# Kernel optimization log

Measured on AMD Instinct MI355X. Metric: run time of the kernel, lower is better.

Reference implementation:

```python
import jax, jax.numpy as jnp
import numpy as np

N = 100000  # nodes

def gcn_layer(x, W, b, src, dst, norm):
    # x: [N, Fin] -> [N, Fout]; symmetric-normalized aggregation (PyG GCNConv)
    h = x @ W                                   # linear first (no bias yet)
    msg = h[src] * norm[:, None]                # gather + edge-wise scale
    out = jax.ops.segment_sum(msg, dst, num_segments=N)  # scatter-add to targets
    return out + b

def _prep_edges(edge_index):
    # add self loops
    loops = jnp.arange(N, dtype=edge_index.dtype)
    src = jnp.concatenate([edge_index[0], loops])
    dst = jnp.concatenate([edge_index[1], loops])
    # deg computed on target nodes with unit edge weights
    deg = jax.ops.segment_sum(jnp.ones_like(dst, dtype=jnp.float32), dst, num_segments=N)
    dinv = jnp.where(deg > 0, jax.lax.rsqrt(deg), 0.0)
    norm = dinv[src] * dinv[dst]
    return src, dst, norm

def setup_inputs() -> dict:
    key = jax.random.key(0)
    ks = jax.random.split(key, 8)
    F_in, H1, H2, C = 512, 256, 64, 10
    E = 3200000
    x = jax.random.normal(ks[0], (N, F_in), dtype=jnp.float32)
    edge_index = jax.random.randint(ks[1], (2, E), 0, N, dtype=jnp.int64)
    def glorot(k, fan_in, fan_out):
        s = jnp.sqrt(6.0 / (fan_in + fan_out))
        return jax.random.uniform(k, (fan_in, fan_out), jnp.float32, -s, s)
    return {
        "x": x,
        "edge_index": edge_index,
        "W1": glorot(ks[2], F_in, H1), "b1": jnp.zeros((H1,), jnp.float32),
        "W2": glorot(ks[3], H1, H2),   "b2": jnp.zeros((H2,), jnp.float32),
        "W3": glorot(ks[4], H2, C),    "b3": jnp.zeros((C,), jnp.float32),
    }

def reference(x, edge_index, W1, b1, W2, b2, W3, b3):
    src, dst, norm = _prep_edges(edge_index)
    h = jax.nn.relu(gcn_layer(x, W1, b1, src, dst, norm))
    h = jax.nn.relu(gcn_layer(h, W2, b2, src, dst, norm))
    h = gcn_layer(h, W3, b3, src, dst, norm)
    return jax.nn.log_softmax(h, axis=1)
```

## Files before the change

### kernel.cpp

```cpp
#include <hip/hip_runtime.h>
#include <math.h>

#define NNODES 100000
#define NEDGES 3200000
#define NB 391
#define PB 512
#define CHUNK 6250

typedef __attribute__((ext_vector_type(4))) float f32x4;
typedef __attribute__((ext_vector_type(2))) float f32x2;
typedef __attribute__((ext_vector_type(8))) short bf16x8;

__device__ __forceinline__ float bf2f(ushort u) {
    union { unsigned u; float f; } v; v.u = ((unsigned)u) << 16; return v.f;
}
__device__ __forceinline__ ushort f2bf(float f) {
    union { float f; unsigned u; } v; v.f = f;
    unsigned r = v.u + 0x7FFFu + ((v.u >> 16) & 1u);
    return (ushort)(r >> 16);
}

__device__ __forceinline__ unsigned pack_bf2(float f0, float f1) {
    union { float f; unsigned u; } a, b; a.f = f0; b.f = f1;
#if __has_builtin(__builtin_amdgcn_perm)
    return __builtin_amdgcn_perm(b.u, a.u, 0x07060302u);
#else
    return (b.u & 0xFFFF0000u) | (a.u >> 16);
#endif
}

#if __has_builtin(__builtin_amdgcn_cvt_pk_fp8_f32) && __has_builtin(__builtin_amdgcn_cvt_pk_f32_fp8)
#define FP8_HW 1
#else
#define FP8_HW 0
#endif

__device__ __forceinline__ unsigned fp8enc_sw(float f) {
    union { float f; unsigned u; } v; v.f = f;
    unsigned sign = v.u >> 31;
    float a = fabsf(f);
    if (a >= 448.0f) return (sign << 7) | 0x7E;
    if (a < 0.0009765625f) return sign << 7;
    unsigned u = v.u & 0x7FFFFFFFu;
    u += 0x7FFFFu + ((u >> 20) & 1u);
    int e2 = (int)(u >> 23) - 127;
    if (e2 < -6) {
        int m = (int)(a * 512.0f + 0.5f); if (m > 7) m = 7;
        return (sign << 7) | (unsigned)m;
    }
    if (e2 > 8) return (sign << 7) | 0x7E;
    unsigned mant = (u >> 20) & 7u;
    return (sign << 7) | ((unsigned)(e2 + 7) << 3) | mant;
}
__device__ __forceinline__ float fp8dec_sw(unsigned b) {
    unsigned s = b >> 7, e = (b >> 3) & 0xF, m = b & 7;
    float v;
    if (e == 0) v = (float)m * 0.001953125f;
    else { union { unsigned u; float f; } x; x.u = ((e + 120u) << 23) | (m << 20); v = x.f; }
    return s ? -v : v;
}

__device__ __forceinline__ unsigned char f2fp8(float f) {
#if FP8_HW
    return (unsigned char)(__builtin_amdgcn_cvt_pk_fp8_f32(f, 0.f, 0, false) & 0xFF);
#else
    return (unsigned char)fp8enc_sw(f);
#endif
}
__device__ __forceinline__ void fp8x4_acc2(unsigned w, f32x2& a01, f32x2& a23) {
#if FP8_HW
    a01 += __builtin_amdgcn_cvt_pk_f32_fp8((int)w, false);
    a23 += __builtin_amdgcn_cvt_pk_f32_fp8((int)w, true);
#else
    a01[0] += fp8dec_sw(w & 0xFF); a01[1] += fp8dec_sw((w >> 8) & 0xFF);
    a23[0] += fp8dec_sw((w >> 16) & 0xFF); a23[1] += fp8dec_sw(w >> 24);
#endif
}

__global__ void bucket_hist(const int* __restrict__ dst, int e, int* __restrict__ hist) {
    __shared__ int h[NB];
    const int b = blockIdx.x, t = threadIdx.x;
    for (int j = t; j < NB; j += 256) h[j] = 0;
    __syncthreads();
    const int lo = b * CHUNK;
    int hi = lo + CHUNK; if (hi > e) hi = e;
    for (int i = lo + t; i < hi; i += 256)
        atomicAdd(&h[dst[i] >> 8], 1);
    __syncthreads();
    for (int j = t; j < NB; j += 256) hist[b * NB + j] = h[j];
}

__global__ void scan_buckets(int* __restrict__ hist, int* __restrict__ btotal) {
    __shared__ int s[256];
    const int j = blockIdx.x, t = threadIdx.x;
    int v0 = hist[(2 * t) * NB + j];
    int v1 = hist[(2 * t + 1) * NB + j];
    int p = v0 + v1;
    s[t] = p;
    __syncthreads();
    for (int off = 1; off < 256; off <<= 1) {
        int u = (t >= off) ? s[t - off] : 0;
        __syncthreads();
        s[t] += u;
        __syncthreads();
    }
    int excl = s[t] - p;
    hist[(2 * t) * NB + j] = excl;
    hist[(2 * t + 1) * NB + j] = excl + v0;
    if (t == 255) btotal[j] = s[255];
}

__global__ void scan_btotal(const int* __restrict__ btotal, int* __restrict__ bstart, int e) {
    __shared__ int s[512];
    const int t = threadIdx.x;
    int v = (t < NB) ? btotal[t] : 0;
    s[t] = v;
    __syncthreads();
    for (int off = 1; off < 512; off <<= 1) {
        int u = (t >= off) ? s[t - off] : 0;
        __syncthreads();
        s[t] += u;
        __syncthreads();
    }
    if (t < NB) bstart[t] = s[t] - v;
    if (t == 0) bstart[NB] = e;
}

__global__ void bucket_scatter(const int* __restrict__ src, const int* __restrict__ dst, int e,
                               const int* __restrict__ hist, const int* __restrict__ bstart,
                               unsigned* __restrict__ bucketed) {
    __shared__ int off[NB];
    const int b = blockIdx.x, t = threadIdx.x;
    for (int j = t; j < NB; j += 256) off[j] = bstart[j] + hist[b * NB + j];
    __syncthreads();
    const int lo = b * CHUNK;
    int hi = lo + CHUNK; if (hi > e) hi = e;
    for (int i = lo + t; i < hi; i += 256) {
        int d = dst[i];
        int j = d >> 8;
        int p = atomicAdd(&off[j], 1);
        bucketed[p] = (unsigned)src[i] | ((unsigned)(d & 255) << 24);
    }
}

__global__ void bucket_finalize(const unsigned* __restrict__ bucketed, const int* __restrict__ bstart,
                                float* __restrict__ dinv, int* __restrict__ rowptr,
                                int* __restrict__ esrc, int n, int e) {
    __shared__ int h[256];
    __shared__ int s[256];
    __shared__ int rp[256];
    const int j = blockIdx.x, t = threadIdx.x;
    h[t] = 0;
    __syncthreads();
    const int lo = bstart[j], hi = bstart[j + 1];
    for (int i = lo + t; i < hi; i += 256)
        atomicAdd(&h[bucketed[i] >> 24], 1);
    __syncthreads();
    const int c = h[t] + 1;
    s[t] = c;
    __syncthreads();
    for (int off = 1; off < 256; off <<= 1) {
        int u = (t >= off) ? s[t - off] : 0;
        __syncthreads();
        s[t] += u;
        __syncthreads();
    }
    const int excl = s[t] - c;
    const int base = j << 8;
    const int node = base + t;
    const int myrp = bstart[j] + base + excl;
    rp[t] = myrp;
    if (node < n) {
        dinv[node] = rsqrtf((float)c);
        rowptr[node] = myrp;
        esrc[myrp] = node;
    }
    if (j == 0 && t == 0) rowptr[n] = e + n;
    h[t] = 0;
    __syncthreads();
    for (int i = lo + t; i < hi; i += 256) {
        unsigned ed = bucketed[i];
        int l = ed >> 24;
        int off = atomicAdd(&h[l], 1);
        esrc[rp[l] + 1 + off] = (int)(ed & 0xFFFFFFu);
    }
}

__global__ void conv_wt(const float* __restrict__ W, ushort* __restrict__ Wt,
                        int K, int N, int Npad) {
    int idx = blockIdx.x * blockDim.x + threadIdx.x;
    if (idx >= Npad * K) return;
    int n = idx / K, k = idx % K;
    Wt[idx] = (n < N) ? f2bf(W[(size_t)k * N + n]) : (ushort)0;
}

__global__ void conv_wt8(const float* __restrict__ W, unsigned char* __restrict__ Wt,
                         int K, int N, int Npad) {
    int idx = blockIdx.x * blockDim.x + threadIdx.x;
    if (idx >= Npad * K) return;
    int n = idx / K, k = idx % K;
    Wt[idx] = (n < N) ? f2fp8(W[(size_t)k * N + n]) : (unsigned char)0;
}

template <int BM, int BN, int BK, int WM, int WN>
__launch_bounds__(WM* WN * 64)
__global__ void gemm_f32a(const float* __restrict__ A, const ushort* __restrict__ Bt,
                          const float* __restrict__ dinv, unsigned char* __restrict__ Cout,
                          int M, int N, int K) {
    constexpr int NT = WM * WN * 64;
    __shared__ __align__(16) float Asf[BM][BK];
    __shared__ __align__(16) ushort Bs[BN][BK];
    const int tid = threadIdx.x;
    const int wid = tid >> 6, lane = tid & 63;
    const int wr = wid / WN, wc = wid % WN;
    constexpr int TM = BM / WM, TN = BN / WN;
    constexpr int FM = TM / 16, FN = TN / 16;
    const int m0 = blockIdx.y * BM, n0 = blockIdx.x * BN;
    const int ln = lane & 15, ks4 = (lane >> 4) * 2;

    f32x4 acc[FM][FN] = {};

    constexpr int CPRA = BK / 4;
    constexpr int ACH = BM * CPRA;
    constexpr int CPRB = BK / 8;
    constexpr int BCH = BN * CPRB;

    for (int k0 = 0; k0 < K; k0 += BK) {
        #pragma unroll
        for (int it = 0; it < ACH / NT; ++it) {
            int c = it * NT + tid;
            int row = c >> 3, chs = c & 7;
            int gch = chs ^ (row & 7);
            int gm = m0 + row; if (gm >= M) gm = M - 1;
            const float* gp = &A[(size_t)gm * K + k0 + gch * 4];
            __builtin_amdgcn_global_load_lds(
                (const __attribute__((address_space(1))) void*)gp,
                (__attribute__((address_space(3))) void*)((char*)&Asf[0][0] + c * 16),
                16, 0, 0);
        }
        #pragma unroll
        for (int it = 0; it < BCH / NT; ++it) {
            int c = it * NT + tid;
            int row = c / CPRB, ch = c % CPRB;
            const ushort* gp = &Bt[(size_t)(n0 + row) * K + k0 + ch * 8];
            __builtin_amdgcn_global_load_lds(
                (const __attribute__((address_space(1))) void*)gp,
                (__attribute__((address_space(3))) void*)((char*)&Bs[0][0] + c * 16),
                16, 0, 0);
        }
        __syncthreads();

        bf16x8 af[FM], bfr[FN];
        #pragma unroll
        for (int mi = 0; mi < FM; ++mi) {
            int r = wr * TM + mi * 16 + ln;
            const char* rowp = (const char*)&Asf[0][0] + r * (BK * 4);
            float4 a0 = *(const float4*)(rowp + ((ks4 ^ (r & 7)) * 16));
            float4 a1 = *(const float4*)(rowp + (((ks4 + 1) ^ (r & 7)) * 16));
            union { unsigned w[4]; bf16x8 v; } u;
            u.w[0] = pack_bf2(a0.x, a0.y);
            u.w[1] = pack_bf2(a0.z, a0.w);
            u.w[2] = pack_bf2(a1.x, a1.y);
            u.w[3] = pack_bf2(a1.z, a1.w);
            af[mi] = u.v;
        }
        const int ks = (lane >> 4) * 8;
        #pragma unroll
        for (int nj = 0; nj < FN; ++nj)
            bfr[nj] = *(const bf16x8*)&Bs[wc * TN + nj * 16 + ln][ks];
        #pragma unroll
        for (int mi = 0; mi < FM; ++mi)
            #pragma unroll
            for (int nj = 0; nj < FN; ++nj)
                acc[mi][nj] = __builtin_amdgcn_mfma_f32_16x16x32_bf16(af[mi], bfr[nj], acc[mi][nj], 0, 0, 0);
        __syncthreads();
    }

    const int rbase = (lane >> 4) * 4;
    #pragma unroll
    for (int mi = 0; mi < FM; ++mi) {
        #pragma unroll
        for (int r = 0; r < 4; ++r) {
            int gm = m0 + wr * TM + mi * 16 + rbase + r;
            if (gm >= M) continue;
            float d = dinv[gm];
            #pragma unroll
            for (int nj = 0; nj < FN; ++nj) {
                int gn = n0 + wc * TN + nj * 16 + ln;
                Cout[(size_t)gm * N + gn] = f2fp8(acc[mi][nj][r] * d);
            }
        }
    }
}

template <int BM, int BN, int BK, int WM, int WN, int OUTK>
__launch_bounds__(WM* WN * 64)
__global__ void gemm_fp8(const unsigned char* __restrict__ A, const unsigned char* __restrict__ Bt,
                         const float* __restrict__ dinv, void* __restrict__ Cout,
                         int M, int N, int K) {
    constexpr int NT = WM * WN * 64;
    __shared__ __align__(16) unsigned char As[BM][BK];
    __shared__ __align__(16) unsigned char Bs[BN][BK];
    const int tid = threadIdx.x;
    const int wid = tid >> 6, lane = tid & 63;
    const int wr = wid / WN, wc = wid % WN;
    constexpr int TM = BM / WM, TN = BN / WN;
    constexpr int FM = TM / 16, FN = TN / 16;
    const int m0 = blockIdx.y * BM, n0 = blockIdx.x * BN;
    const int ln = lane & 15;

    f32x4 acc[FM][FN] = {};

    constexpr int CPR = BK / 16;
    constexpr int ACH = BM * CPR;
    constexpr int BCH = BN * CPR;

    for (int k0 = 0; k0 < K; k0 += BK) {
        #pragma unroll
        for (int it = 0; it < (ACH + NT - 1) / NT; ++it) {
            int c = it * NT + tid;
            if ((ACH % NT == 0) || (c < ACH)) {
                int row = c / CPR, ch = c % CPR;
                int gm = m0 + row; if (gm >= M) gm = M - 1;
                const unsigned char* gp = &A[(size_t)gm * K + k0 + ch * 16];
                __builtin_amdgcn_global_load_lds(
                    (const __attribute__((address_space(1))) void*)gp,
                    (__attribute__((address_space(3))) void*)((char*)&As[0][0] + c * 16),
                    16, 0, 0);
            }
        }
        #pragma unroll
        for (int it = 0; it < (BCH + NT - 1) / NT; ++it) {
            int c = it * NT + tid;
            if ((BCH % NT == 0) || (c < BCH)) {
                int row = c / CPR, ch = c % CPR;
                const unsigned char* gp = &Bt[(size_t)(n0 + row) * K + k0 + ch * 16];
                __builtin_amdgcn_global_load_lds(
                    (const __attribute__((address_space(1))) void*)gp,
                    (__attribute__((address_space(3))) void*)((char*)&Bs[0][0] + c * 16),
                    16, 0, 0);
            }
        }
        __syncthreads();

        long af[FM], bfr[FN];
        #pragma unroll
        for (int mi = 0; mi < FM; ++mi)
            af[mi] = ((const long*)&As[0][0])[(wr * TM + mi * 16 + ln) * (BK / 8) + (lane >> 4)];
        #pragma unroll
        for (int nj = 0; nj < FN; ++nj)
            bfr[nj] = ((const long*)&Bs[0][0])[(wc * TN + nj * 16 + ln) * (BK / 8) + (lane >> 4)];
        #pragma unroll
        for (int mi = 0; mi < FM; ++mi)
            #pragma unroll
            for (int nj = 0; nj < FN; ++nj)
                acc[mi][nj] = __builtin_amdgcn_mfma_f32_16x16x32_fp8_fp8(af[mi], bfr[nj], acc[mi][nj], 0, 0, 0);
        __syncthreads();
    }

    const int rbase = (lane >> 4) * 4;
    #pragma unroll
    for (int mi = 0; mi < FM; ++mi) {
        #pragma unroll
        for (int r = 0; r < 4; ++r) {
            int gm = m0 + wr * TM + mi * 16 + rbase + r;
            if (gm >= M) continue;
            float d = dinv[gm];
            #pragma unroll
            for (int nj = 0; nj < FN; ++nj) {
                int gn = n0 + wc * TN + nj * 16 + ln;
                float v = acc[mi][nj][r] * d;
                if (OUTK == 0) ((ushort*)Cout)[(size_t)gm * N + gn] = f2bf(v);
                else           ((unsigned char*)Cout)[(size_t)gm * N + gn] = f2fp8(v);
            }
        }
    }
}

__global__ void agg1_fp8(const unsigned* __restrict__ h, const int* __restrict__ rowptr,
                         const int* __restrict__ esrc, const float* __restrict__ dinv,
                         const float* __restrict__ bias, unsigned char* __restrict__ out, int n) {
    const int wid = threadIdx.x >> 6, lane = threadIdx.x & 63;
    const int i = blockIdx.x * 4 + wid;
    if (i >= n) return;
    const int lo = rowptr[i], hi = rowptr[i + 1];
    f32x2 a01 = {0.f, 0.f}, a23 = {0.f, 0.f};
    int e = lo;
    for (; e + 7 < hi; e += 8) {
        int s[8];
        unsigned w[8];
        #pragma unroll
        for (int q = 0; q < 8; ++q) s[q] = esrc[e + q];
        #pragma unroll
        for (int q = 0; q < 8; ++q) w[q] = h[(size_t)s[q] * 64 + lane];
        #pragma unroll
        for (int q = 0; q < 8; ++q) fp8x4_acc2(w[q], a01, a23);
    }
    for (; e < hi; ++e)
        fp8x4_acc2(h[(size_t)esrc[e] * 64 + lane], a01, a23);

    float d = dinv[i];
    const int f0 = lane * 4;
    float4 b = *(const float4*)&bias[f0];
    uchar4 o;
    o.x = f2fp8(fmaxf(a01[0] * d + b.x, 0.f));
    o.y = f2fp8(fmaxf(a01[1] * d + b.y, 0.f));
    o.z = f2fp8(fmaxf(a23[0] * d + b.z, 0.f));
    o.w = f2fp8(fmaxf(a23[1] * d + b.w, 0.f));
    *(uchar4*)&out[(size_t)i * 256 + f0] = o;
}

__global__ void agg2_fp8(const unsigned* __restrict__ h, const int* __restrict__ rowptr,
                         const int* __restrict__ esrc, const float* __restrict__ dinv,
                         const float* __restrict__ bias, unsigned char* __restrict__ out, int n) {
    const int g = threadIdx.x >> 4, j = threadIdx.x & 15;
    const int i = blockIdx.x * 16 + g;
    if (i >= n) return;
    const int lo = rowptr[i], hi = rowptr[i + 1];
    f32x2 a01 = {0.f, 0.f}, a23 = {0.f, 0.f};
    int e = lo;
    for (; e + 3 < hi; e += 4) {
        int s0 = esrc[e], s1 = esrc[e + 1], s2 = esrc[e + 2], s3 = esrc[e + 3];
        unsigned w0 = h[(size_t)s0 * 16 + j];
        unsigned w1 = h[(size_t)s1 * 16 + j];
        unsigned w2 = h[(size_t)s2 * 16 + j];
        unsigned w3 = h[(size_t)s3 * 16 + j];
        fp8x4_acc2(w0, a01, a23);
        fp8x4_acc2(w1, a01, a23);
        fp8x4_acc2(w2, a01, a23);
        fp8x4_acc2(w3, a01, a23);
    }
    for (; e < hi; ++e)
        fp8x4_acc2(h[(size_t)esrc[e] * 16 + j], a01, a23);

    float d = dinv[i];
    const int f0 = j * 4;
    float4 b = *(const float4*)&bias[f0];
    uchar4 o;
    o.x = f2fp8(fmaxf(a01[0] * d + b.x, 0.f));
    o.y = f2fp8(fmaxf(a01[1] * d + b.y, 0.f));
    o.z = f2fp8(fmaxf(a23[0] * d + b.z, 0.f));
    o.w = f2fp8(fmaxf(a23[1] * d + b.w, 0.f));
    *(uchar4*)&out[(size_t)i * 64 + f0] = o;
}

__global__ void agg3_logsoftmax(const ushort* __restrict__ h3, const int* __restrict__ rowptr,
                                const int* __restrict__ esrc, const float* __restrict__ dinv,
                                const float* __restrict__ bias, float* __restrict__ out, int n) {
    const int g = threadIdx.x >> 3, j = threadIdx.x & 7;
    const int i = blockIdx.x * 32 + g;
    if (i >= n) return;
    const int lo = rowptr[i], hi = rowptr[i + 1];
    float a0 = 0.f, a1 = 0.f;
    int e = lo;
    for (; e + 3 < hi; e += 4) {
        int s0 = esrc[e], s1 = esrc[e + 1], s2 = esrc[e + 2], s3 = esrc[e + 3];
        unsigned w0 = *(const unsigned*)&h3[(size_t)s0 * 16 + 2 * j];
        unsigned w1 = *(const unsigned*)&h3[(size_t)s1 * 16 + 2 * j];
        unsigned w2 = *(const unsigned*)&h3[(size_t)s2 * 16 + 2 * j];
        unsigned w3 = *(const unsigned*)&h3[(size_t)s3 * 16 + 2 * j];
        a0 += bf2f((ushort)(w0 & 0xFFFF)) + bf2f((ushort)(w1 & 0xFFFF))
            + bf2f((ushort)(w2 & 0xFFFF)) + bf2f((ushort)(w3 & 0xFFFF));
        a1 += bf2f((ushort)(w0 >> 16)) + bf2f((ushort)(w1 >> 16))
            + bf2f((ushort)(w2 >> 16)) + bf2f((ushort)(w3 >> 16));
    }
    for (; e < hi; ++e) {
        unsigned w = *(const unsigned*)&h3[(size_t)esrc[e] * 16 + 2 * j];
        a0 += bf2f((ushort)(w & 0xFFFF));
        a1 += bf2f((ushort)(w >> 16));
    }
    const int f0 = 2 * j;
    float d = dinv[i];
    float v0 = (f0 < 10) ? (a0 * d + bias[f0]) : -INFINITY;
    float v1 = (f0 + 1 < 10) ? (a1 * d + bias[f0 + 1]) : -INFINITY;
    float m = fmaxf(v0, v1);
    #pragma unroll
    for (int off = 1; off < 8; off <<= 1) m = fmaxf(m, __shfl_xor(m, off, 8));
    float ex = ((f0 < 10) ? expf(v0 - m) : 0.f) + ((f0 + 1 < 10) ? expf(v1 - m) : 0.f);
    #pragma unroll
    for (int off = 1; off < 8; off <<= 1) ex += __shfl_xor(ex, off, 8);
    float ls = logf(ex);
    if (f0 < 10)     out[(size_t)i * 10 + f0] = v0 - m - ls;
    if (f0 + 1 < 10) out[(size_t)i * 10 + f0 + 1] = v1 - m - ls;
}

extern "C" void kernel_launch(void* const* d_in, const int* in_sizes, int n_in,
                              void* d_out, int out_size, void* d_ws, size_t ws_size,
                              hipStream_t stream) {
    const int N = NNODES, E = NEDGES;
    const float* x  = (const float*)d_in[0];
    const int*   ei = (const int*)d_in[1];
    const float* W1 = (const float*)d_in[2];
    const float* b1 = (const float*)d_in[3];
    const float* W2 = (const float*)d_in[4];
    const float* b2 = (const float*)d_in[5];
    const float* W3 = (const float*)d_in[6];
    const float* b3 = (const float*)d_in[7];
    float* out = (float*)d_out;
    const int* src = ei;
    const int* dst = ei + E;

    char* ws = (char*)d_ws;
    size_t off = 0;
    auto alloc = [&](size_t bytes) -> void* {
        void* p = ws + off;
        off = (off + bytes + 255) & ~(size_t)255;
        return p;
    };
    float* dinv   = (float*)alloc((size_t)N * 4);
    int*   rowptr = (int*)alloc((size_t)(N + 1) * 4);
    int*   btotal = (int*)alloc((size_t)NB * 4);
    int*   bstart = (int*)alloc((size_t)(NB + 1) * 4);
    int*   esrc   = (int*)alloc((size_t)(E + N) * 4);
    ushort* W1t   = (ushort*)alloc((size_t)256 * 512 * 2);
    unsigned char* W2t8 = (unsigned char*)alloc((size_t)64 * 256);
    unsigned char* W3t8 = (unsigned char*)alloc((size_t)16 * 64);
    ushort* h3b   = (ushort*)alloc((size_t)N * 16 * 2);
    ushort* buf1  = (ushort*)alloc((size_t)N * 256 * 2);
    ushort* buf2  = (ushort*)alloc((size_t)N * 256 * 2);
    int*   hist   = (int*)buf1;
    unsigned* bucketed = (unsigned*)buf2;
    unsigned char* h1fp8 = (unsigned char*)buf1;
    unsigned char* a1fp8 = (unsigned char*)buf2;
    unsigned char* h2fp8 = (unsigned char*)buf1;
    unsigned char* a2fp8 = (unsigned char*)buf2;

    const int T = 256;
    bucket_hist<<<PB, T, 0, stream>>>(dst, E, hist);
    scan_buckets<<<NB, T, 0, stream>>>(hist, btotal);
    scan_btotal<<<1, 512, 0, stream>>>(btotal, bstart, E);
    bucket_scatter<<<PB, T, 0, stream>>>(src, dst, E, hist, bstart, bucketed);
    bucket_finalize<<<NB, T, 0, stream>>>(bucketed, bstart, dinv, rowptr, esrc, N, E);

    conv_wt<<<(256 * 512 + T - 1) / T, T, 0, stream>>>(W1, W1t, 512, 256, 256);
    conv_wt8<<<(64 * 256 + T - 1) / T, T, 0, stream>>>(W2, W2t8, 256, 64, 64);
    conv_wt8<<<(16 * 64 + T - 1) / T, T, 0, stream>>>(W3, W3t8, 64, 10, 16);

    const int MB = (N + 127) / 128;

    gemm_f32a<128, 256, 32, 2, 4><<<dim3(1, MB), 512, 0, stream>>>(x, W1t, dinv, h1fp8, N, 256, 512);
    agg1_fp8<<<(N + 3) / 4, 256, 0, stream>>>((const unsigned*)h1fp8, rowptr, esrc, dinv, b1, a1fp8, N);

    gemm_fp8<128, 64, 32, 2, 2, 2><<<dim3(1, MB), 256, 0, stream>>>(a1fp8, W2t8, dinv, h2fp8, N, 64, 256);
    agg2_fp8<<<(N + 15) / 16, 256, 0, stream>>>((const unsigned*)h2fp8, rowptr, esrc, dinv, b2, a2fp8, N);

    gemm_fp8<128, 16, 32, 4, 1, 0><<<dim3(1, MB), 256, 0, stream>>>(a2fp8, W3t8, dinv, h3b, N, 16, 64);
    agg3_logsoftmax<<<(N + 31) / 32, 256, 0, stream>>>(h3b, rowptr, esrc, dinv, b3, out, N);
}
```

Measured before the change: 382.5 us.

## Split layer-1 aggregation into feature halves with edge-parallel lanes per wave

The layer-1 aggregation kernel now launches twice as many blocks. Each wave handles one node and one 128-feature half. The two 32-lane halves of the wave process alternate edges and combine their sums with a cross-lane shuffle. Blocks are ordered so that adjacent blocks cover both halves of the same node group, which aims to narrow the gather footprint per pass and improve L2 locality of the 256-byte rows. The layer-2 aggregation loop is unrolled from 4 to 8 edges, and the two small weight-conversion kernels are merged into one launch. The new grid uses N/4 without rounding up, which only covers every node because N is divisible by 4. The extra shuffle and the duplicated index loads add overhead.

New measurement: 408.2 us. 6.7% more time.

```diff
diff --git a/kernel.cpp b/kernel.cpp
--- a/kernel.cpp
+++ b/kernel.cpp
@@ -194,12 +194,17 @@
     Wt[idx] = (n < N) ? f2bf(W[(size_t)k * N + n]) : (ushort)0;
 }
 
-__global__ void conv_wt8(const float* __restrict__ W, unsigned char* __restrict__ Wt,
-                         int K, int N, int Npad) {
+__global__ void conv_w23(const float* __restrict__ W2, unsigned char* __restrict__ W2t,
+                         const float* __restrict__ W3, unsigned char* __restrict__ W3t) {
     int idx = blockIdx.x * blockDim.x + threadIdx.x;
-    if (idx >= Npad * K) return;
-    int n = idx / K, k = idx % K;
-    Wt[idx] = (n < N) ? f2fp8(W[(size_t)k * N + n]) : (unsigned char)0;
+    if (idx < 64 * 256) {
+        int n = idx / 256, k = idx % 256;
+        W2t[idx] = f2fp8(W2[(size_t)k * 64 + n]);
+    } else if (idx < 64 * 256 + 16 * 64) {
+        int r = idx - 64 * 256;
+        int n = r / 64, k = r % 64;
+        W3t[r] = (n < 10) ? f2fp8(W3[(size_t)k * 10 + n]) : (unsigned char)0;
+    }
 }
 
 template <int BM, int BN, int BK, int WM, int WN>
@@ -380,34 +385,49 @@
 __global__ void agg1_fp8(const unsigned* __restrict__ h, const int* __restrict__ rowptr,
                          const int* __restrict__ esrc, const float* __restrict__ dinv,
                          const float* __restrict__ bias, unsigned char* __restrict__ out, int n) {
+    const int bid = blockIdx.x;
+    const int g8 = bid & 7;
+    const int half = g8 >> 2;
+    const int seq = (bid >> 3) * 4 + (g8 & 3);
     const int wid = threadIdx.x >> 6, lane = threadIdx.x & 63;
-    const int i = blockIdx.x * 4 + wid;
+    const int i = seq * 4 + wid;
     if (i >= n) return;
     const int lo = rowptr[i], hi = rowptr[i + 1];
+    const int lh = lane & 31;
+    const int eo = lane >> 5;
+    const unsigned* hh = h + half * 32 + lh;
     f32x2 a01 = {0.f, 0.f}, a23 = {0.f, 0.f};
-    int e = lo;
-    for (; e + 7 < hi; e += 8) {
-        int s[8];
-        unsigned w[8];
-        #pragma unroll
-        for (int q = 0; q < 8; ++q) s[q] = esrc[e + q];
-        #pragma unroll
-        for (int q = 0; q < 8; ++q) w[q] = h[(size_t)s[q] * 64 + lane];
-        #pragma unroll
-        for (int q = 0; q < 8; ++q) fp8x4_acc2(w[q], a01, a23);
-    }
-    for (; e < hi; ++e)
-        fp8x4_acc2(h[(size_t)esrc[e] * 64 + lane], a01, a23);
-
-    float d = dinv[i];
-    const int f0 = lane * 4;
-    float4 b = *(const float4*)&bias[f0];
-    uchar4 o;
-    o.x = f2fp8(fmaxf(a01[0] * d + b.x, 0.f));
-    o.y = f2fp8(fmaxf(a01[1] * d + b.y, 0.f));
-    o.z = f2fp8(fmaxf(a23[0] * d + b.z, 0.f));
-    o.w = f2fp8(fmaxf(a23[1] * d + b.w, 0.f));
-    *(uchar4*)&out[(size_t)i * 256 + f0] = o;
+    int e = lo + eo;
+    for (; e + 6 < hi; e += 8) {
+        int s0 = esrc[e], s1 = esrc[e + 2], s2 = esrc[e + 4], s3 = esrc[e + 6];
+        unsigned w0 = hh[(size_t)s0 * 64];
+        unsigned w1 = hh[(size_t)s1 * 64];
+        unsigned w2 = hh[(size_t)s2 * 64];
+        unsigned w3 = hh[(size_t)s3 * 64];
+        fp8x4_acc2(w0, a01, a23);
+        fp8x4_acc2(w1, a01, a23);
+        fp8x4_acc2(w2, a01, a23);
+        fp8x4_acc2(w3, a01, a23);
+    }
+    for (; e < hi; e += 2)
+        fp8x4_acc2(hh[(size_t)esrc[e] * 64], a01, a23);
+
+    a01[0] += __shfl_xor(a01[0], 32);
+    a01[1] += __shfl_xor(a01[1], 32);
+    a23[0] += __shfl_xor(a23[0], 32);
+    a23[1] += __shfl_xor(a23[1], 32);
+
+    if (lane < 32) {
+        float d = dinv[i];
+        const int f0 = half * 128 + lh * 4;
+        float4 b = *(const float4*)&bias[f0];
+        uchar4 o;
+        o.x = f2fp8(fmaxf(a01[0] * d + b.x, 0.f));
+        o.y = f2fp8(fmaxf(a01[1] * d + b.y, 0.f));
+        o.z = f2fp8(fmaxf(a23[0] * d + b.z, 0.f));
+        o.w = f2fp8(fmaxf(a23[1] * d + b.w, 0.f));
+        *(uchar4*)&out[(size_t)i * 256 + f0] = o;
+    }
 }
 
 __global__ void agg2_fp8(const unsigned* __restrict__ h, const int* __restrict__ rowptr,
@@ -419,16 +439,15 @@
     const int lo = rowptr[i], hi = rowptr[i + 1];
     f32x2 a01 = {0.f, 0.f}, a23 = {0.f, 0.f};
     int e = lo;
-    for (; e + 3 < hi; e += 4) {
-        int s0 = esrc[e], s1 = esrc[e + 1], s2 = esrc[e + 2], s3 = esrc[e + 3];
-        unsigned w0 = h[(size_t)s0 * 16 + j];
-        unsigned w1 = h[(size_t)s1 * 16 + j];
-        unsigned w2 = h[(size_t)s2 * 16 + j];
-        unsigned w3 = h[(size_t)s3 * 16 + j];
-        fp8x4_acc2(w0, a01, a23);
-        fp8x4_acc2(w1, a01, a23);
-        fp8x4_acc2(w2, a01, a23);
-        fp8x4_acc2(w3, a01, a23);
+    for (; e + 7 < hi; e += 8) {
+        int s[8];
+        unsigned w[8];
+        #pragma unroll
+        for (int q = 0; q < 8; ++q) s[q] = esrc[e + q];
+        #pragma unroll
+        for (int q = 0; q < 8; ++q) w[q] = h[(size_t)s[q] * 16 + j];
+        #pragma unroll
+        for (int q = 0; q < 8; ++q) fp8x4_acc2(w[q], a01, a23);
     }
     for (; e < hi; ++e)
         fp8x4_acc2(h[(size_t)esrc[e] * 16 + j], a01, a23);
@@ -533,13 +552,12 @@
     bucket_finalize<<<NB, T, 0, stream>>>(bucketed, bstart, dinv, rowptr, esrc, N, E);
 
     conv_wt<<<(256 * 512 + T - 1) / T, T, 0, stream>>>(W1, W1t, 512, 256, 256);
-    conv_wt8<<<(64 * 256 + T - 1) / T, T, 0, stream>>>(W2, W2t8, 256, 64, 64);
-    conv_wt8<<<(16 * 64 + T - 1) / T, T, 0, stream>>>(W3, W3t8, 64, 10, 16);
+    conv_w23<<<(64 * 256 + 16 * 64 + T - 1) / T, T, 0, stream>>>(W2, W2t8, W3, W3t8);
 
     const int MB = (N + 127) / 128;
 
     gemm_f32a<128, 256, 32, 2, 4><<<dim3(1, MB), 512, 0, stream>>>(x, W1t, dinv, h1fp8, N, 256, 512);
-    agg1_fp8<<<(N + 3) / 4, 256, 0, stream>>>((const unsigned*)h1fp8, rowptr, esrc, dinv, b1, a1fp8, N);
+    agg1_fp8<<<2 * (N / 4), 256, 0, stream>>>((const unsigned*)h1fp8, rowptr, esrc, dinv, b1, a1fp8, N);
 
     gemm_fp8<128, 64, 32, 2, 2, 2><<<dim3(1, MB), 256, 0, stream>>>(a1fp8, W2t8, dinv, h2fp8, N, 64, 256);
     agg2_fp8<<<(N + 15) / 16, 256, 0, stream>>>((const unsigned*)h2fp8, rowptr, esrc, dinv, b2, a2fp8, N);
```
